# Optimization experiments

Measured on AMD Instinct MI355X. Metric: run time of the kernel, lower is better.

Reference implementation:

```python
import jax, jax.numpy as jnp
import numpy as np

SCALE = 64.0
MARGIN = 0.35
LAMBDA = 0.4
GAMMA = 2
EPS = 1e-12


def _l2_normalize(v, axis=-1):
    n = jnp.sqrt(jnp.sum(v * v, axis=axis, keepdims=True))
    return v / jnp.maximum(n, EPS)


def setup_inputs() -> dict:
    key = jax.random.key(0)
    k1, k2, k3, k4 = jax.random.split(key, 4)
    B, D, C = 1024, 512, 100000
    stdv = 1.0 / np.sqrt(D)
    x = jax.random.normal(k1, (B, D), dtype=jnp.float32)
    target = jax.random.randint(k2, (B,), 0, C, dtype=jnp.int64)
    id_agent = jax.random.uniform(k3, (C, D), dtype=jnp.float32, minval=-stdv, maxval=stdv)
    b = jax.random.uniform(k4, (C, D), dtype=jnp.float32, minval=-stdv, maxval=stdv)
    return {"x": x, "target": target, "id_agent": id_agent, "b": b}


def reference(x, target, id_agent, b):
    B = x.shape[0]
    x_n = _l2_normalize(x, axis=1)              # [B, D]
    w = _l2_normalize(id_agent, axis=1)         # [C, D] (in-place normalize in torch)

    # discriminative loss
    w_batch = w[target]                          # [B, D] gather
    d = x_n - w_batch                            # displacement vectors
    bt = b[target]                               # [B, D]
    bt_norm = jnp.sqrt(jnp.sum(bt * bt, axis=1, keepdims=True))
    bt_norm_c = jnp.clip(bt_norm, 0.0, 0.05)
    bt_unit = bt / jnp.maximum(bt_norm, EPS)
    resid = d - bt_unit * bt_norm_c
    loss_disc = jnp.mean(jnp.sqrt(jnp.sum(resid * resid, axis=1)))

    # AM-softmax logits with margin on target class (training mode)
    score = x_n @ w.T                            # [B, C] large GEMM
    rows = jnp.arange(B)
    score = score.at[rows, target].add(-MARGIN)
    score = score * SCALE

    # focal cross-entropy: CE mean first, then focal modulation (as in source)
    logsm = jax.nn.log_softmax(score, axis=1)
    nll = -logsm[rows, target]
    logp = jnp.mean(nll)
    p = jnp.exp(-logp)
    loss_score = (1.0 - p) ** GAMMA * logp

    return (LAMBDA * loss_disc + loss_score)[None]  # shape [1]
```

## Files before the change

### kernel.cpp

```cpp
#include <hip/hip_runtime.h>
#include <hip/hip_bf16.h>

typedef __attribute__((ext_vector_type(4))) int i32x4;

#define B_N 1024
#define D_K 512
#define C_N 100000
#define SCALE_F 64.0f
#define MARGIN_F 0.35f
#define BM 128
#define BN 256
#define BKB 128
#define NT_ 391
#define MT_ 8
#define WBLKS 25000
#define MAXL 64.0f
#define LOG2E 1.4426950408889634f
#define KQ2 (SCALE_F / (127.0f * 127.0f) * LOG2E)
#define MAXL2 (MAXL * LOG2E)

__device__ __forceinline__ float dot4(float4 a, float4 b) {
    return a.x * b.x + a.y * b.y + a.z * b.z + a.w * b.w;
}
__device__ __forceinline__ float amax4(float4 a) {
    return fmaxf(fmaxf(fabsf(a.x), fabsf(a.y)), fmaxf(fabsf(a.z), fabsf(a.w)));
}
__device__ __forceinline__ int packq(float v0, float v1, float v2, float v3, float qs) {
    int q0 = __float2int_rn(v0 * qs), q1 = __float2int_rn(v1 * qs);
    int q2 = __float2int_rn(v2 * qs), q3 = __float2int_rn(v3 * qs);
    return (q0 & 0xFF) | ((q1 & 0xFF) << 8) | ((q2 & 0xFF) << 16) | ((q3 & 0xFF) << 24);
}

__global__ void prep_kernel(const float* __restrict__ x,
                            const int* __restrict__ target,
                            const float* __restrict__ ida,
                            const float* __restrict__ bmat,
                            char* __restrict__ xq,
                            float* __restrict__ sx,
                            char* __restrict__ wq,
                            float* __restrict__ sw,
                            float* __restrict__ dpart,
                            float* __restrict__ tlogit,
                            float* __restrict__ rowsum) {
    int blk = blockIdx.x;
    int wave = threadIdx.x >> 6;
    int l = threadIdx.x & 63;

    if (blk < WBLKS) {
        int row = blk * 4 + wave;
        const float4* rp = (const float4*)(ida + (size_t)row * D_K);
        float4 a = rp[l], b = rp[64 + l];
        float ssq = dot4(a, a) + dot4(b, b);
        float mx = fmaxf(amax4(a), amax4(b));
#pragma unroll
        for (int m = 1; m < 64; m <<= 1) {
            ssq += __shfl_xor(ssq, m);
            mx = fmaxf(mx, __shfl_xor(mx, m));
        }
        float inv = 1.0f / fmaxf(sqrtf(ssq), 1e-12f);
        float swm = fmaxf(mx * inv, 1e-12f);
        float qs = 127.0f / swm * inv;
        int* oq = (int*)(wq + (size_t)row * D_K);
        oq[l] = packq(a.x, a.y, a.z, a.w, qs);
        oq[64 + l] = packq(b.x, b.y, b.z, b.w, qs);
        if (l == 0) sw[row] = swm;
        return;
    }

    int row = (blk - WBLKS) * 4 + wave;
    long t = (long)target[row];
    const float4* xp = (const float4*)(x + (size_t)row * D_K);
    const float4* wp = (const float4*)(ida + (size_t)t * D_K);
    const float4* bp = (const float4*)(bmat + (size_t)t * D_K);
    float4 x0 = xp[l], x1 = xp[64 + l];
    float4 w0 = wp[l], w1 = wp[64 + l];
    float4 b0 = bp[l], b1 = bp[64 + l];
    float xssq = dot4(x0, x0) + dot4(x1, x1);
    float wssq = dot4(w0, w0) + dot4(w1, w1);
    float bssq = dot4(b0, b0) + dot4(b1, b1);
    float xmx = fmaxf(amax4(x0), amax4(x1));
#pragma unroll
    for (int m = 1; m < 64; m <<= 1) {
        xssq += __shfl_xor(xssq, m);
        wssq += __shfl_xor(wssq, m);
        bssq += __shfl_xor(bssq, m);
        xmx = fmaxf(xmx, __shfl_xor(xmx, m));
    }
    float xinv = 1.0f / fmaxf(sqrtf(xssq), 1e-12f);
    float winv = 1.0f / fmaxf(sqrtf(wssq), 1e-12f);
    float btn = sqrtf(bssq);
    float cs = fminf(btn, 0.05f) / fmaxf(btn, 1e-12f);

    float sxm = fmaxf(xmx * xinv, 1e-12f);
    float qs = 127.0f / sxm * xinv;
    int* oq = (int*)(xq + (size_t)row * D_K);
    oq[l] = packq(x0.x, x0.y, x0.z, x0.w, qs);
    oq[64 + l] = packq(x1.x, x1.y, x1.z, x1.w, qs);

    float xs[8] = {x0.x, x0.y, x0.z, x0.w, x1.x, x1.y, x1.z, x1.w};
    float wv[8] = {w0.x, w0.y, w0.z, w0.w, w1.x, w1.y, w1.z, w1.w};
    float bv[8] = {b0.x, b0.y, b0.z, b0.w, b1.x, b1.y, b1.z, b1.w};
    float rss = 0.0f, dt = 0.0f;
#pragma unroll
    for (int i = 0; i < 8; ++i) {
        float xn = xs[i] * xinv;
        float wn = wv[i] * winv;
        float d = xn - wn;
        float r = d - bv[i] * cs;
        rss += r * r;
        dt += xn * wn;
    }
#pragma unroll
    for (int m = 1; m < 64; m <<= 1) {
        rss += __shfl_xor(rss, m);
        dt += __shfl_xor(dt, m);
    }
    if (l == 0) {
        sx[row] = sxm;
        dpart[row] = sqrtf(rss);
        tlogit[row] = SCALE_F * dt;
        rowsum[row] = 0.0f;
    }
}

__global__ __launch_bounds__(512, 4) void gemm_lse_kernel(const char* __restrict__ A,
                                                          const char* __restrict__ W,
                                                          const float* __restrict__ sx,
                                                          const float* __restrict__ sw,
                                                          float* __restrict__ rowsum) {
    __shared__ char As[BM * BKB];
    __shared__ char Bs[BN * BKB];
    __shared__ float sxl[BM];
    __shared__ float swl[BN];
    __shared__ float rs[4][BM];

    int tid = threadIdx.x;
    int wave = tid >> 6, l = tid & 63;
    int wm = wave >> 2, wn = wave & 3;

    int wgid = (blockIdx.x & 7) * NT_ + (blockIdx.x >> 3);
    int nt = wgid >> 3, mt = wgid & 7;
    int m0 = mt * BM, n0 = nt * BN;

    int srow = l >> 3;
    int scolB = ((l & 7) ^ (l >> 3)) * 16;

    {
        if (tid < BN) {
            int c = n0 + tid;
            swl[tid] = (c < C_N) ? sw[c] : 0.0f;
        } else if (tid < BN + BM) {
            sxl[tid - BN] = sx[m0 + tid - BN];
        }
    }

    const char* aBase = A + (size_t)(m0 + wave * 16 + srow) * D_K + scolB;
    const char* bBase[4];
#pragma unroll
    for (int i = 0; i < 4; ++i) {
        int rn = n0 + wave * 32 + i * 8 + srow;
        rn = rn < C_N ? rn : C_N - 1;
        bBase[i] = W + (size_t)rn * D_K + scolB;
    }

    i32x4 acc[4][4];
#pragma unroll
    for (int i = 0; i < 4; ++i)
#pragma unroll
        for (int j = 0; j < 4; ++j) acc[i][j] = (i32x4){0, 0, 0, 0};

    int cl = l & 15, hi = l >> 4;

#pragma unroll
    for (int kt = 0; kt < 4; ++kt) {
#pragma unroll
        for (int i = 0; i < 2; ++i)
            __builtin_amdgcn_global_load_lds(
                (const __attribute__((address_space(1))) void*)(aBase + i * (8 * D_K) + kt * BKB),
                (__attribute__((address_space(3))) void*)&As[(wave * 16 + i * 8) * BKB], 16, 0, 0);
#pragma unroll
        for (int i = 0; i < 4; ++i)
            __builtin_amdgcn_global_load_lds(
                (const __attribute__((address_space(1))) void*)(bBase[i] + kt * BKB),
                (__attribute__((address_space(3))) void*)&Bs[(wave * 32 + i * 8) * BKB], 16, 0, 0);
        __syncthreads();

#pragma unroll
        for (int kk = 0; kk < 2; ++kk) {
            int px = (((kk << 2) | hi) ^ (cl & 7)) * 16;
            i32x4 af[4], bfr[4];
#pragma unroll
            for (int mi = 0; mi < 4; ++mi)
                af[mi] = *(const i32x4*)&As[(wm * 64 + mi * 16 + cl) * BKB + px];
#pragma unroll
            for (int ni = 0; ni < 4; ++ni)
                bfr[ni] = *(const i32x4*)&Bs[(wn * 64 + ni * 16 + cl) * BKB + px];
#pragma unroll
            for (int mi = 0; mi < 4; ++mi)
#pragma unroll
                for (int ni = 0; ni < 4; ++ni)
                    acc[mi][ni] = __builtin_amdgcn_mfma_i32_16x16x64_i8(af[mi], bfr[ni], acc[mi][ni], 0, 0, 0);
        }
        __syncthreads();
    }

    float fcv[4];
#pragma unroll
    for (int ni = 0; ni < 4; ++ni)
        fcv[ni] = swl[wn * 64 + ni * 16 + cl];

#pragma unroll
    for (int mi = 0; mi < 4; ++mi) {
#pragma unroll
        for (int j = 0; j < 4; ++j) {
            float fr = sxl[wm * 64 + mi * 16 + hi * 4 + j] * KQ2;
            float se = 0.0f;
#pragma unroll
            for (int ni = 0; ni < 4; ++ni)
                se += exp2f((float)acc[mi][ni][j] * fr * fcv[ni] - MAXL2);
#pragma unroll
            for (int xm = 1; xm < 16; xm <<= 1) se += __shfl_xor(se, xm);
            if (cl == 0) rs[wn][wm * 64 + mi * 16 + hi * 4 + j] = se;
        }
    }
    __syncthreads();
    if (tid < BM) {
        float s = rs[0][tid] + rs[1][tid] + rs[2][tid] + rs[3][tid];
        atomicAdd(&rowsum[m0 + tid], s);
    }
}

__global__ void rowfin_final_kernel(const float* __restrict__ rowsum,
                                    const float* __restrict__ tlogit,
                                    const float* __restrict__ dpart,
                                    float* __restrict__ out) {
    __shared__ float redn[16];
    __shared__ float redd[16];
    int tid = threadIdx.x;
    float lse = MAXL + logf(rowsum[tid]);
    float st = tlogit[tid];
    float corr = __expf(st - lse) * (__expf(-SCALE_F * MARGIN_F) - 1.0f);
    float lse2 = lse + log1pf(corr);
    float nll = lse2 - (st - SCALE_F * MARGIN_F);
    float dv = dpart[tid];
#pragma unroll
    for (int xm = 1; xm < 64; xm <<= 1) {
        nll += __shfl_xor(nll, xm);
        dv += __shfl_xor(dv, xm);
    }
    if ((tid & 63) == 0) {
        redn[tid >> 6] = nll;
        redd[tid >> 6] = dv;
    }
    __syncthreads();
    if (tid == 0) {
        float sn = 0.0f, sd = 0.0f;
#pragma unroll
        for (int i = 0; i < 16; ++i) { sn += redn[i]; sd += redd[i]; }
        float logp = sn * (1.0f / B_N);
        float disc = sd * (1.0f / B_N);
        float p = __expf(-logp);
        float om = 1.0f - p;
        out[0] = 0.4f * disc + om * om * logp;
    }
}

extern "C" void kernel_launch(void* const* d_in, const int* in_sizes, int n_in,
                              void* d_out, int out_size, void* d_ws, size_t ws_size,
                              hipStream_t stream) {
    const float* x = (const float*)d_in[0];
    const int* target = (const int*)d_in[1];
    const float* ida = (const float*)d_in[2];
    const float* bmat = (const float*)d_in[3];
    float* out = (float*)d_out;

    char* ws = (char*)d_ws;
    size_t off = 0;
    float* rowsum = (float*)(ws + off);  off += (size_t)B_N * 4;
    char* xq = (char*)(ws + off);        off += (size_t)B_N * D_K;
    char* wq = (char*)(ws + off);        off += (size_t)C_N * D_K;
    float* sx = (float*)(ws + off);      off += (size_t)B_N * 4;
    float* sw = (float*)(ws + off);      off += (size_t)C_N * 4;
    float* tlogit = (float*)(ws + off);  off += (size_t)B_N * 4;
    float* dpart = (float*)(ws + off);   off += (size_t)B_N * 4;

    prep_kernel<<<WBLKS + B_N / 4, 256, 0, stream>>>(x, target, ida, bmat, xq, sx,
                                                     wq, sw, dpart, tlogit, rowsum);
    gemm_lse_kernel<<<MT_ * NT_, 512, 0, stream>>>(xq, wq, sx, sw, rowsum);
    rowfin_final_kernel<<<1, 1024, 0, stream>>>(rowsum, tlogit, dpart, out);
}
```

Baseline: 134.4 us.

## Double-buffer LDS tiles in int8 GEMM to overlap loads with MFMA

Splits the shared-memory A and B tiles into two buffers. The next K-slice is issued by asynchronous global-to-LDS loads while MFMAs run on the current buffer, and the four-step K loop is unrolled by hand, with one barrier per step instead of two. The goal is to hide global load latency inside each workgroup. In exchange LDS use per block roughly doubles and launch bounds drop from 4 to 2 blocks per CU, which lowers occupancy and the overlap that used to come from running several workgroups at once.

```diff
diff --git a/kernel.cpp b/kernel.cpp
--- a/kernel.cpp
+++ b/kernel.cpp
@@ -123,13 +123,13 @@
     }
 }
 
-__global__ __launch_bounds__(512, 4) void gemm_lse_kernel(const char* __restrict__ A,
+__global__ __launch_bounds__(512, 2) void gemm_lse_kernel(const char* __restrict__ A,
                                                           const char* __restrict__ W,
                                                           const float* __restrict__ sx,
                                                           const float* __restrict__ sw,
                                                           float* __restrict__ rowsum) {
-    __shared__ char As[BM * BKB];
-    __shared__ char Bs[BN * BKB];
+    __shared__ char As[2][BM * BKB];
+    __shared__ char Bs[2][BN * BKB];
     __shared__ float sxl[BM];
     __shared__ float swl[BN];
     __shared__ float rs[4][BM];
@@ -163,6 +163,17 @@
         bBase[i] = W + (size_t)rn * D_K + scolB;
     }
 
+#define GLL(SRC, DST) __builtin_amdgcn_global_load_lds(                          \
+        (const __attribute__((address_space(1))) void*)(SRC),                    \
+        (__attribute__((address_space(3))) void*)(DST), 16, 0, 0)
+#define STG(KT, BUF) do {                                                        \
+    _Pragma("unroll") for (int i_ = 0; i_ < 2; ++i_)                             \
+        GLL(aBase + i_ * (8 * D_K) + (KT) * BKB,                                 \
+            &As[BUF][(wave * 16 + i_ * 8) * BKB]);                               \
+    _Pragma("unroll") for (int i_ = 0; i_ < 4; ++i_)                             \
+        GLL(bBase[i_] + (KT) * BKB,                                              \
+            &Bs[BUF][(wave * 32 + i_ * 8) * BKB]); } while (0)
+
     i32x4 acc[4][4];
 #pragma unroll
     for (int i = 0; i < 4; ++i)
@@ -171,38 +182,25 @@
 
     int cl = l & 15, hi = l >> 4;
 
-#pragma unroll
-    for (int kt = 0; kt < 4; ++kt) {
-#pragma unroll
-        for (int i = 0; i < 2; ++i)
-            __builtin_amdgcn_global_load_lds(
-                (const __attribute__((address_space(1))) void*)(aBase + i * (8 * D_K) + kt * BKB),
-                (__attribute__((address_space(3))) void*)&As[(wave * 16 + i * 8) * BKB], 16, 0, 0);
-#pragma unroll
-        for (int i = 0; i < 4; ++i)
-            __builtin_amdgcn_global_load_lds(
-                (const __attribute__((address_space(1))) void*)(bBase[i] + kt * BKB),
-                (__attribute__((address_space(3))) void*)&Bs[(wave * 32 + i * 8) * BKB], 16, 0, 0);
-        __syncthreads();
-
-#pragma unroll
-        for (int kk = 0; kk < 2; ++kk) {
-            int px = (((kk << 2) | hi) ^ (cl & 7)) * 16;
-            i32x4 af[4], bfr[4];
-#pragma unroll
-            for (int mi = 0; mi < 4; ++mi)
-                af[mi] = *(const i32x4*)&As[(wm * 64 + mi * 16 + cl) * BKB + px];
-#pragma unroll
-            for (int ni = 0; ni < 4; ++ni)
-                bfr[ni] = *(const i32x4*)&Bs[(wn * 64 + ni * 16 + cl) * BKB + px];
-#pragma unroll
-            for (int mi = 0; mi < 4; ++mi)
-#pragma unroll
-                for (int ni = 0; ni < 4; ++ni)
-                    acc[mi][ni] = __builtin_amdgcn_mfma_i32_16x16x64_i8(af[mi], bfr[ni], acc[mi][ni], 0, 0, 0);
-        }
-        __syncthreads();
-    }
+#define COMP(BUF) do {                                                           \
+    _Pragma("unroll") for (int kk = 0; kk < 2; ++kk) {                           \
+        int px = (((kk << 2) | hi) ^ (cl & 7)) * 16;                             \
+        i32x4 af[4], bfr[4];                                                     \
+        _Pragma("unroll") for (int mi = 0; mi < 4; ++mi)                         \
+            af[mi] = *(const i32x4*)&As[BUF][(wm * 64 + mi * 16 + cl) * BKB + px]; \
+        _Pragma("unroll") for (int ni = 0; ni < 4; ++ni)                         \
+            bfr[ni] = *(const i32x4*)&Bs[BUF][(wn * 64 + ni * 16 + cl) * BKB + px]; \
+        _Pragma("unroll") for (int mi = 0; mi < 4; ++mi)                         \
+            _Pragma("unroll") for (int ni = 0; ni < 4; ++ni)                     \
+                acc[mi][ni] = __builtin_amdgcn_mfma_i32_16x16x64_i8(af[mi], bfr[ni], acc[mi][ni], 0, 0, 0); \
+    } } while (0)
+
+    STG(0, 0);
+    __syncthreads();
+    STG(1, 1); COMP(0); __syncthreads();
+    STG(2, 0); COMP(1); __syncthreads();
+    STG(3, 1); COMP(0); __syncthreads();
+    COMP(1);
 
     float fcv[4];
 #pragma unroll
@@ -228,6 +226,9 @@
         float s = rs[0][tid] + rs[1][tid] + rs[2][tid] + rs[3][tid];
         atomicAdd(&rowsum[m0 + tid], s);
     }
+#undef GLL
+#undef STG
+#undef COMP
 }
 
 __global__ void rowfin_final_kernel(const float* __restrict__ rowsum,
```

Result: slower. 163.8 us (+21.9%).
